# Performance work log

Measured on AMD Instinct MI355X. Metric: run time of the kernel, lower is better.

The kernel has to match this reference:

```python
import jax, jax.numpy as jnp
import numpy as np
from jax import lax

BN_EPS = 1e-5
LEAKY_RATE = 0.1
SPECTRAL_RADIUS = 0.99


def _bn_eval(x, gamma, beta, mean, var):
    # x: (B, F, ...); params: (F,) broadcast over trailing dims
    shape = (1, -1) + (1,) * (x.ndim - 2)
    inv = gamma.reshape(shape) / jnp.sqrt(var.reshape(shape) + BN_EPS)
    return (x - mean.reshape(shape)) * inv + beta.reshape(shape)


def setup_inputs() -> dict:
    key = jax.random.key(0)
    ks = jax.random.split(key, 12)
    B, C, T, F, H, NCLS = 32, 72, 1000, 64, 512, 3
    x = jax.random.normal(ks[0], (B, 1, C, T), dtype=jnp.float32)
    w_temp = jax.random.normal(ks[1], (F, 1, 1, 5), dtype=jnp.float32) * 0.1
    bn1_gamma = jnp.ones((F,), jnp.float32)
    bn1_beta = jnp.zeros((F,), jnp.float32)
    bn1_mean = jax.random.normal(ks[2], (F,), dtype=jnp.float32) * 0.1
    bn1_var = jax.random.uniform(ks[3], (F,), dtype=jnp.float32) + 0.5
    w_spatial = jax.random.normal(ks[4], (F, C), dtype=jnp.float32) * 0.1
    bn2_gamma = jnp.ones((F,), jnp.float32)
    bn2_beta = jnp.zeros((F,), jnp.float32)
    bn2_mean = jax.random.normal(ks[5], (F,), dtype=jnp.float32) * 0.1
    bn2_var = jax.random.uniform(ks[6], (F,), dtype=jnp.float32) + 0.5
    w_in = jax.random.normal(ks[7], (H, F), dtype=jnp.float32) * (1.0 / np.sqrt(F))
    b_in = jax.random.normal(ks[8], (H,), dtype=jnp.float32) * 0.1
    # reservoir weight: uniform(-0.5, 0.5) scaled to spectral norm = 0.99 (frozen in torch)
    W = jax.random.uniform(ks[9], (H, H), dtype=jnp.float32, minval=-0.5, maxval=0.5)
    W = W * (SPECTRAL_RADIUS / jnp.linalg.norm(W, ord=2))
    w_cls = jax.random.normal(ks[10], (NCLS, H), dtype=jnp.float32) * (1.0 / np.sqrt(H))
    b_cls = jax.random.normal(ks[11], (NCLS,), dtype=jnp.float32) * 0.1
    return dict(x=x, w_temp=w_temp, bn1_gamma=bn1_gamma, bn1_beta=bn1_beta,
                bn1_mean=bn1_mean, bn1_var=bn1_var, w_spatial=w_spatial,
                bn2_gamma=bn2_gamma, bn2_beta=bn2_beta, bn2_mean=bn2_mean,
                bn2_var=bn2_var, w_in=w_in, b_in=b_in, W=W, w_cls=w_cls, b_cls=b_cls)


def _forward(x, w_temp, bn1_gamma, bn1_beta, bn1_mean, bn1_var, w_spatial,
             bn2_gamma, bn2_beta, bn2_mean, bn2_var, w_in, b_in, W, w_cls, b_cls):
    # temporal conv: (B,1,C,T) -> (B,F,C,T), kernel (1,5), pad (0,2)
    out = lax.conv_general_dilated(x, w_temp, window_strides=(1, 1),
                                   padding=((0, 0), (2, 2)),
                                   dimension_numbers=('NCHW', 'OIHW', 'NCHW'))
    out = jax.nn.elu(_bn_eval(out, bn1_gamma, bn1_beta, bn1_mean, bn1_var))
    # depthwise spatial conv over full channel height: (B,F,C,T) x (F,C) -> (B,F,T)
    out = jnp.einsum('bfct,fc->bft', out, w_spatial)
    out = jax.nn.elu(_bn_eval(out, bn2_gamma, bn2_beta, bn2_mean, bn2_var))
    feats = jnp.swapaxes(out, 1, 2)  # (B, T, F)
    # ESN: precompute input projection, scan the nonlinear recurrence over time
    u_in = jnp.einsum('btf,hf->bth', feats, w_in) + b_in  # (B,T,H)
    B, T, H = u_in.shape
    a = LEAKY_RATE

    def step(h, u_t):
        h_new = (1.0 - a) * h + a * jnp.tanh(u_t + h @ W.T)
        return h_new, h_new

    h0 = jnp.zeros((B, H), u_in.dtype)
    _, hs = lax.scan(step, h0, jnp.swapaxes(u_in, 0, 1))  # hs: (T,B,H)
    pooled = hs.mean(axis=0)  # mean over time (dropout is identity at eval)
    return pooled @ w_cls.T + b_cls  # (B, n_classes)


def reference(x, w_temp, bn1_gamma, bn1_beta, bn1_mean, bn1_var, w_spatial,
              bn2_gamma, bn2_beta, bn2_mean, bn2_var, w_in, b_in, W, w_cls, b_cls):
    return _forward(x, w_temp, bn1_gamma, bn1_beta, bn1_mean, bn1_var, w_spatial,
                    bn2_gamma, bn2_beta, bn2_mean, bn2_var, w_in, b_in, W, w_cls, b_cls)
```

## Files before the change

kernel.cpp:

```cpp
#include <hip/hip_runtime.h>
#include <math.h>

#define NB 32
#define NC 72
#define NT 1000
#define NF 64
#define NH 512
#define NCLS 3

#define OFF_FEATS   0
#define OFF_POOLED  2048000
#define OFF_HX      2064384
#define WS_FLOATS   2129920

#define HIDX2(k) ((k) + (((k) >> 5) << 2))
#define HPAD (NH + 64)

__global__ void prep_kernel(unsigned long long* __restrict__ hx) {
  int i = blockIdx.x * 256 + threadIdx.x;
  if (i < 2 * NB * NH) hx[i] = 0ull;
}

__global__ __launch_bounds__(256) void frontend_kernel(
    const float* __restrict__ x, const float* __restrict__ w_temp,
    const float* __restrict__ g1, const float* __restrict__ be1,
    const float* __restrict__ m1, const float* __restrict__ v1,
    const float* __restrict__ wsp,
    const float* __restrict__ g2, const float* __restrict__ be2,
    const float* __restrict__ m2, const float* __restrict__ v2,
    float* __restrict__ feats) {
  const int b = blockIdx.y;
  const int t0 = blockIdx.x * 64;

  __shared__ float xs[NC][68];
  for (int idx = threadIdx.x; idx < NC * 68; idx += 256) {
    int c = idx / 68, tt = idx % 68;
    int tg = t0 - 2 + tt;
    xs[c][tt] = (tg >= 0 && tg < NT) ? x[(b * NC + c) * NT + tg] : 0.0f;
  }
  __syncthreads();

  const int f = threadIdx.x & 63;
  const int tq = threadIdx.x >> 6;

  const float w0 = w_temp[f * 5 + 0], w1 = w_temp[f * 5 + 1], w2 = w_temp[f * 5 + 2],
              w3 = w_temp[f * 5 + 3], w4 = w_temp[f * 5 + 4];
  const float sc1 = g1[f] * rsqrtf(v1[f] + 1e-5f);
  const float sh1 = be1[f] - m1[f] * sc1;
  const float sc2 = g2[f] * rsqrtf(v2[f] + 1e-5f);
  const float sh2 = be2[f] - m2[f] * sc2;

  for (int i = 0; i < 16; ++i) {
    const int tl = tq + 4 * i;
    const int t = t0 + tl;
    if (t >= NT) break;
    float acc = 0.0f;
    for (int c = 0; c < NC; ++c) {
      const float* xr = &xs[c][tl];
      float conv = xr[0] * w0 + xr[1] * w1 + xr[2] * w2 + xr[3] * w3 + xr[4] * w4;
      float bn = conv * sc1 + sh1;
      float e = bn > 0.0f ? bn : __expf(bn) - 1.0f;
      acc += e * wsp[f * NC + c];
    }
    float bn2 = acc * sc2 + sh2;
    float e2 = bn2 > 0.0f ? bn2 : __expf(bn2) - 1.0f;
    feats[(b * NT + t) * NF + f] = e2;
  }
}

__global__ __launch_bounds__(512, 1) void esn_scan(
    const float* __restrict__ Wm, const float* __restrict__ w_in,
    const float* __restrict__ b_in, const float* __restrict__ feats,
    unsigned long long* __restrict__ hx, float* __restrict__ pooled) {
  const int b = blockIdx.x & 31;
  const int m = blockIdx.x >> 5;
  const int tid = threadIdx.x;
  const int grp = tid >> 4;
  const int p = tid & 15;
  const int c0 = m * 128 + grp * 4;

  __shared__ __align__(16) float h2[2][HPAD];
  __shared__ __align__(16) float f2[2][NF];

  float w[4][32];
#pragma unroll
  for (int c = 0; c < 4; ++c)
#pragma unroll
    for (int i = 0; i < 32; i += 4) {
      float4 t = *(const float4*)&Wm[(c0 + c) * NH + p * 32 + i];
      w[c][i] = t.x; w[c][i + 1] = t.y; w[c][i + 2] = t.z; w[c][i + 3] = t.w;
    }
#pragma unroll
  for (int c = 0; c < 4; ++c)
#pragma unroll
    for (int i = 0; i < 32; ++i) asm volatile("" : "+v"(w[c][i]));

  float wu[4][4];
#pragma unroll
  for (int c = 0; c < 4; ++c) {
    float4 t = *(const float4*)&w_in[(c0 + c) * NF + p * 4];
    wu[c][0] = t.x; wu[c][1] = t.y; wu[c][2] = t.z; wu[c][3] = t.w;
  }
  float be[4];
  {
    float4 bv = *(const float4*)&b_in[c0];
    be[0] = p == 0 ? bv.x : 0.0f; be[1] = p == 0 ? bv.y : 0.0f;
    be[2] = p == 0 ? bv.z : 0.0f; be[3] = p == 0 ? bv.w : 0.0f;
  }

  for (int i = tid; i < HPAD; i += 512) h2[0][i] = 0.0f;
  if (tid < NF) f2[0][tid] = feats[(b * NT) * NF + tid];
  __syncthreads();

  float* hc = &h2[0][0];
  float* hb = &h2[1][0];
  float* fc = &f2[0][0];
  float* fb = &f2[1][0];

  float pool = 0.0f;
  int budget = 20000000;

#pragma unroll 1
  for (int t = 0; t < NT; ++t) {
    float acc[4] = {be[0], be[1], be[2], be[3]};
    {
      float4 fv = *(const float4*)&fc[p * 4];
#pragma unroll
      for (int c = 0; c < 4; ++c)
        acc[c] += fv.x * wu[c][0] + fv.y * wu[c][1] + fv.z * wu[c][2] + fv.w * wu[c][3];
    }
#pragma unroll
    for (int i = 0; i < 8; ++i) {
      float4 hv = *(const float4*)&hc[p * 36 + i * 4];
#pragma unroll
      for (int c = 0; c < 4; ++c)
        acc[c] += hv.x * w[c][i * 4] + hv.y * w[c][i * 4 + 1] +
                  hv.z * w[c][i * 4 + 2] + hv.w * w[c][i * 4 + 3];
    }
#pragma unroll
    for (int c = 0; c < 4; ++c) {
      acc[c] += __shfl_xor(acc[c], 1);
      acc[c] += __shfl_xor(acc[c], 2);
      acc[c] += __shfl_xor(acc[c], 4);
      acc[c] += __shfl_xor(acc[c], 8);
    }

    unsigned long long* hxb = hx + ((t + 1) & 1) * (NB * NH) + b * NH;
    if (p < 4) {
      const int j = c0 + p;
      float asel = p == 0 ? acc[0] : p == 1 ? acc[1] : p == 2 ? acc[2] : acc[3];
      float hn = 0.9f * hc[HIDX2(j)] + 0.1f * tanhf(asel);
      pool += hn;
      if (t < NT - 1) {
        unsigned long long pk =
            ((unsigned long long)(unsigned)(t + 1) << 32) | (unsigned)__float_as_uint(hn);
        __hip_atomic_store(&hxb[j], pk, __ATOMIC_RELAXED, __HIP_MEMORY_SCOPE_AGENT);
        hb[HIDX2(j)] = hn;
      }
    }
    if (t == NT - 1) break;

    float fnext = 0.0f;
    if (tid < NF) fnext = feats[(b * NT + t + 1) * NF + tid];

    const int k = tid;
    if ((k >> 7) != m) {
      unsigned long long q;
      for (;;) {
        q = __hip_atomic_load(&hxb[k], __ATOMIC_RELAXED, __HIP_MEMORY_SCOPE_AGENT);
        if ((unsigned)(q >> 32) == (unsigned)(t + 1)) break;
        if (--budget < 0) break;
        __builtin_amdgcn_s_sleep(1);
      }
      hb[HIDX2(k)] = __uint_as_float((unsigned)q);
    }
    if (tid < NF) fb[tid] = fnext;
    __syncthreads();
    { float* tp = hc; hc = hb; hb = tp; }
    { float* tp = fc; fc = fb; fb = tp; }
  }

  if (p < 4) pooled[b * NH + c0 + p] = pool * (1.0f / NT);
}

__global__ void classifier_kernel(const float* __restrict__ pooled,
                                  const float* __restrict__ w_cls,
                                  const float* __restrict__ b_cls,
                                  float* __restrict__ out) {
  const int b = blockIdx.x;
  const int lane = threadIdx.x;
  float a0 = 0.0f, a1 = 0.0f, a2 = 0.0f;
  for (int jj = lane; jj < NH; jj += 64) {
    float pv = pooled[b * NH + jj];
    a0 += pv * w_cls[0 * NH + jj];
    a1 += pv * w_cls[1 * NH + jj];
    a2 += pv * w_cls[2 * NH + jj];
  }
  for (int off = 32; off; off >>= 1) {
    a0 += __shfl_down(a0, off);
    a1 += __shfl_down(a1, off);
    a2 += __shfl_down(a2, off);
  }
  if (lane == 0) {
    out[b * NCLS + 0] = a0 + b_cls[0];
    out[b * NCLS + 1] = a1 + b_cls[1];
    out[b * NCLS + 2] = a2 + b_cls[2];
  }
}

extern "C" void kernel_launch(void* const* d_in, const int* in_sizes, int n_in,
                              void* d_out, int out_size, void* d_ws, size_t ws_size,
                              hipStream_t stream) {
  (void)in_sizes; (void)n_in; (void)out_size;
  if (ws_size < (size_t)WS_FLOATS * 4) return;

  const float* x      = (const float*)d_in[0];
  const float* w_temp = (const float*)d_in[1];
  const float* g1  = (const float*)d_in[2];
  const float* be1 = (const float*)d_in[3];
  const float* m1  = (const float*)d_in[4];
  const float* v1  = (const float*)d_in[5];
  const float* wsp = (const float*)d_in[6];
  const float* g2  = (const float*)d_in[7];
  const float* be2 = (const float*)d_in[8];
  const float* m2  = (const float*)d_in[9];
  const float* v2  = (const float*)d_in[10];
  const float* w_in  = (const float*)d_in[11];
  const float* b_in  = (const float*)d_in[12];
  const float* Wm    = (const float*)d_in[13];
  const float* w_cls = (const float*)d_in[14];
  const float* b_cls = (const float*)d_in[15];

  float* ws_f  = (float*)d_ws;
  float* feats = ws_f + OFF_FEATS;
  float* pooledp = ws_f + OFF_POOLED;
  unsigned long long* hx = (unsigned long long*)(ws_f + OFF_HX);

  prep_kernel<<<128, 256, 0, stream>>>(hx);

  dim3 gfe(16, NB);
  frontend_kernel<<<gfe, 256, 0, stream>>>(x, w_temp, g1, be1, m1, v1, wsp,
                                           g2, be2, m2, v2, feats);

  esn_scan<<<128, 512, 0, stream>>>(Wm, w_in, b_in, feats, hx, pooledp);

  classifier_kernel<<<NB, 64, 0, stream>>>(pooledp, w_cls, b_cls, (float*)d_out);
}
```

Before: 1.693 ms.

## Pipeline cross-block polling loads and hoist feature prefetch in ESN scan

The spin-wait for peer hidden-state values now issues five staggered inline-asm global loads with short sleeps between them, then checks each result in order as it arrives, so a freshly published value is seen sooner than with one load followed by a sleep. The next feature row is fetched at the start of each step to hide its latency behind the matvec. The block-wide __syncthreads is replaced by a raw s_barrier preceded by an explicit LDS wait. This adds more in-flight memory traffic while polling, and the retry budget is lowered, which raises the chance of reading a stale value under heavy contention.

```diff
diff --git a/kernel.cpp b/kernel.cpp
--- a/kernel.cpp
+++ b/kernel.cpp
@@ -118,10 +118,14 @@
   float* fb = &f2[1][0];
 
   float pool = 0.0f;
-  int budget = 20000000;
+  int budget = 200000;
+  unsigned long long a0 = 0, a1 = 0, a2 = 0, a3 = 0, a4 = 0;
 
 #pragma unroll 1
   for (int t = 0; t < NT; ++t) {
+    float fnext = 0.0f;
+    if (tid < NF && t < NT - 1) fnext = feats[(b * NT + t + 1) * NF + tid];
+
     float acc[4] = {be[0], be[1], be[2], be[3]};
     {
       float4 fv = *(const float4*)&fc[p * 4];
@@ -145,7 +149,8 @@
       acc[c] += __shfl_xor(acc[c], 8);
     }
 
-    unsigned long long* hxb = hx + ((t + 1) & 1) * (NB * NH) + b * NH;
+    const int par = (t + 1) & 1;
+    unsigned long long* hxb = hx + par * (NB * NH) + b * NH;
     if (p < 4) {
       const int j = c0 + p;
       float asel = p == 0 ? acc[0] : p == 1 ? acc[1] : p == 2 ? acc[2] : acc[3];
@@ -160,25 +165,62 @@
     }
     if (t == NT - 1) break;
 
-    float fnext = 0.0f;
-    if (tid < NF) fnext = feats[(b * NT + t + 1) * NF + tid];
+    if (tid < NF) fb[tid] = fnext;
 
     const int k = tid;
     if ((k >> 7) != m) {
-      unsigned long long q;
-      for (;;) {
-        q = __hip_atomic_load(&hxb[k], __ATOMIC_RELAXED, __HIP_MEMORY_SCOPE_AGENT);
-        if ((unsigned)(q >> 32) == (unsigned)(t + 1)) break;
-        if (--budget < 0) break;
-        __builtin_amdgcn_s_sleep(1);
+      const unsigned e = (unsigned)(t + 1);
+      const unsigned long long* ap = &hxb[k];
+      unsigned long long qv = 0;
+      bool got = false;
+      while (!got && --budget >= 0) {
+        asm volatile("global_load_dwordx2 %0, %1, off sc1" : "=v"(a0) : "v"(ap));
+        __builtin_amdgcn_s_sleep(6);
+        asm volatile("global_load_dwordx2 %0, %1, off sc1" : "=v"(a1) : "v"(ap));
+        __builtin_amdgcn_s_sleep(6);
+        asm volatile("global_load_dwordx2 %0, %1, off sc1" : "=v"(a2) : "v"(ap));
+        __builtin_amdgcn_s_sleep(6);
+        asm volatile("global_load_dwordx2 %0, %1, off sc1" : "=v"(a3) : "v"(ap));
+        __builtin_amdgcn_s_sleep(6);
+        asm volatile("global_load_dwordx2 %0, %1, off sc1" : "=v"(a4) : "v"(ap));
+        asm volatile("s_waitcnt vmcnt(4)" ::: "memory");
+        __builtin_amdgcn_sched_barrier(0);
+        if ((unsigned)(a0 >> 32) == e) { qv = a0; got = true; }
+        if (!got) {
+          asm volatile("s_waitcnt vmcnt(3)" ::: "memory");
+          __builtin_amdgcn_sched_barrier(0);
+          if ((unsigned)(a1 >> 32) == e) { qv = a1; got = true; }
+        }
+        if (!got) {
+          asm volatile("s_waitcnt vmcnt(2)" ::: "memory");
+          __builtin_amdgcn_sched_barrier(0);
+          if ((unsigned)(a2 >> 32) == e) { qv = a2; got = true; }
+        }
+        if (!got) {
+          asm volatile("s_waitcnt vmcnt(1)" ::: "memory");
+          __builtin_amdgcn_sched_barrier(0);
+          if ((unsigned)(a3 >> 32) == e) { qv = a3; got = true; }
+        }
+        if (!got) {
+          asm volatile("s_waitcnt vmcnt(0)" ::: "memory");
+          __builtin_amdgcn_sched_barrier(0);
+          if ((unsigned)(a4 >> 32) == e) { qv = a4; got = true; }
+        }
       }
-      hb[HIDX2(k)] = __uint_as_float((unsigned)q);
-    }
-    if (tid < NF) fb[tid] = fnext;
-    __syncthreads();
+      hb[HIDX2(k)] = __uint_as_float((unsigned)qv);
+    }
+
+    asm volatile("s_waitcnt lgkmcnt(0)" ::: "memory");
+    __builtin_amdgcn_sched_barrier(0);
+    __builtin_amdgcn_s_barrier();
+    __builtin_amdgcn_sched_barrier(0);
+
     { float* tp = hc; hc = hb; hb = tp; }
     { float* tp = fc; fc = fb; fb = tp; }
   }
+
+  asm volatile("s_waitcnt vmcnt(0)" ::: "memory");
+  asm volatile("" :: "v"(a0), "v"(a1), "v"(a2), "v"(a3), "v"(a4));
 
   if (p < 4) pooled[b * NH + c0 + p] = pool * (1.0f / NT);
 }
```

Measured after the change: 2.212 ms. 30.6% more time.
